# Optimization experiments

Measured on AMD Instinct MI355X. Metric: run time of the kernel, lower is better.

The kernel has to match this reference:

```python
import jax, jax.numpy as jnp
import numpy as np

KERNEL_BW = 0.4  # RBF (Laplacian) kernel bandwidth from the original code


def setup_inputs() -> dict:
    key = jax.random.key(0)
    k1, k2 = jax.random.split(key)
    N, C = 8192, 1000
    inp = jax.random.normal(k1, (N, C), dtype=jnp.float32)
    target = jax.random.randint(k2, (N,), 0, C, dtype=jnp.int64)
    return {"input": inp, "target": target}


def reference(input, target):
    # input: [N, C] logits; target: [N] int labels
    target = target.reshape(-1)
    probs = jax.nn.softmax(input, axis=1)
    predicted_probs = jnp.max(probs, axis=1)           # [N] confidence p_i
    pred_labels = jnp.argmax(probs, axis=1)            # [N]
    correct_mask = (pred_labels == target).astype(predicted_probs.dtype)  # [N]
    c_minus_r = correct_mask - predicted_probs          # [N]
    # Pairwise terms: dot[i,j] = (c_i - p_i)(c_j - p_j); k[i,j] = exp(-|p_i - p_j| / 0.4)
    dot_product = jnp.outer(c_minus_r, c_minus_r)       # [N, N]
    kernel = jnp.exp(-jnp.abs(predicted_probs[:, None] - predicted_probs[None, :]) / KERNEL_BW)
    n = predicted_probs.shape[0]
    return jnp.sum(dot_product * kernel) / jnp.asarray(n, predicted_probs.dtype) ** 2
```

## Files before the change

### kernel.cpp

```cpp
#include <hip/hip_runtime.h>
#include <math.h>
#include <stdint.h>


#define WAVE 64
static constexpr float KBW_INV = 2.5f;

__global__ __launch_bounds__(256) void rowstats_kernel(
    const float* __restrict__ inp, const int* __restrict__ tgt,
    float* __restrict__ P, float* __restrict__ A, float* __restrict__ B,
    int N, int C) {
  const int wave = threadIdx.x >> 6;
  const int lane = threadIdx.x & 63;
  const int row = blockIdx.x * 4 + wave;
  if (row >= N) return;
  const int C4 = C >> 2;
  const float4* rp = reinterpret_cast<const float4*>(inp + (size_t)row * C);

  float4 x[4];
  bool valid[4];
  float m = -INFINITY;
  int am = 0x7fffffff;
  #pragma unroll
  for (int w = 0; w < 4; ++w) {
    const int k = lane + w * WAVE;
    valid[w] = (k < C4);
    if (valid[w]) {
      float4 v = rp[k];
      x[w] = v;
      const int base = k * 4;
      if (v.x > m) { m = v.x; am = base + 0; }
      if (v.y > m) { m = v.y; am = base + 1; }
      if (v.z > m) { m = v.z; am = base + 2; }
      if (v.w > m) { m = v.w; am = base + 3; }
    }
  }
  #pragma unroll
  for (int off = 32; off; off >>= 1) {
    float om = __shfl_xor(m, off);
    int oi = __shfl_xor(am, off);
    if (om > m || (om == m && oi < am)) { m = om; am = oi; }
  }
  float s = 0.f;
  #pragma unroll
  for (int w = 0; w < 4; ++w) {
    if (valid[w]) {
      s += __expf(x[w].x - m) + __expf(x[w].y - m) +
           __expf(x[w].z - m) + __expf(x[w].w - m);
    }
  }
  #pragma unroll
  for (int off = 32; off; off >>= 1) s += __shfl_xor(s, off);

  if (lane == 0) {
    const float p = 1.0f / s;
    const float v = ((tgt[row] == am) ? 1.0f : 0.0f) - p;
    P[row] = p;
    A[row] = v * __expf(-p * KBW_INV);
    B[row] = v * __expf(p * KBW_INV);
  }
}

#define JBLK 256

__global__ __launch_bounds__(256) void pairwise_kernel(
    const float* __restrict__ P, const float* __restrict__ A,
    const float* __restrict__ B, double* __restrict__ partials, int N) {
  __shared__ float sp[JBLK], sa[JBLK], sb[JBLK];
  const int nIB = N / 256;
  const int bi = blockIdx.x % nIB;
  const int bj = blockIdx.x / nIB;
  const int tid = threadIdx.x;

  const int j = bj * JBLK + tid;
  sp[tid] = P[j];
  sa[tid] = A[j];
  sb[tid] = B[j];
  __syncthreads();

  const int i = bi * 256 + tid;
  const float pi = P[i];
  const float ai = A[i];
  const float bi_ = B[i];
  double acc = 0.0;
  #pragma unroll 8
  for (int t = 0; t < JBLK; ++t) {
    const float pj = sp[t];
    const bool c = (pi >= pj);
    const float xx = c ? ai : bi_;
    const float yy = c ? sb[t] : sa[t];
    acc += (double)(xx * yy);
  }
  #pragma unroll
  for (int off = 32; off; off >>= 1) acc += __shfl_xor(acc, off);
  __shared__ double wsum[4];
  if ((tid & 63) == 0) wsum[tid >> 6] = acc;
  __syncthreads();
  if (tid == 0) partials[blockIdx.x] = (wsum[0] + wsum[1]) + (wsum[2] + wsum[3]);
}

__global__ __launch_bounds__(256) void finalize_kernel(
    const double* __restrict__ partials, int nPart, float* __restrict__ out,
    double invN2) {
  double acc = 0.0;
  for (int k = threadIdx.x; k < nPart; k += 256) acc += partials[k];
  #pragma unroll
  for (int off = 32; off; off >>= 1) acc += __shfl_xor(acc, off);
  __shared__ double wsum[4];
  if ((threadIdx.x & 63) == 0) wsum[threadIdx.x >> 6] = acc;
  __syncthreads();
  if (threadIdx.x == 0)
    out[0] = (float)(((wsum[0] + wsum[1]) + (wsum[2] + wsum[3])) * invN2);
}

extern "C" void kernel_launch(void* const* d_in, const int* in_sizes, int n_in,
                              void* d_out, int out_size, void* d_ws, size_t ws_size,
                              hipStream_t stream) {
  const float* inp = (const float*)d_in[0];
  const int* tgt = (const int*)d_in[1];
  const int N = in_sizes[1];
  const int C = in_sizes[0] / N;

  float* P = (float*)d_ws;
  float* A = P + N;
  float* B = A + N;
  double* partials =
      (double*)(((uintptr_t)(B + N) + 15) & ~(uintptr_t)15);

  const int rowBlocks = (N + 3) / 4;
  rowstats_kernel<<<rowBlocks, 256, 0, stream>>>(inp, tgt, P, A, B, N, C);

  const int nIB = N / 256;
  const int nPart = nIB * nIB;
  pairwise_kernel<<<nPart, 256, 0, stream>>>(P, A, B, partials, N);

  finalize_kernel<<<1, 256, 0, stream>>>(partials, nPart, (float*)d_out,
                                         1.0 / ((double)N * (double)N));
}
```

Before: 29.40 us.

## Replace pairwise compare-select with fmed3, register-block rows, fuse finalize via atomics

The pairwise kernel no longer loads P. It uses the identity that min(a_i*b_j, b_i*a_j), clamped against zero via fmed3, selects the correct exp term, and accumulates in float instead of double per term. Each thread now handles 4 rows against 128-column tiles from a packed float2 A/B array. The finalize kernel is removed in favour of a fixed-point 64-bit atomic accumulate with a last-block counter. This cuts double-precision adds, loads and one launch, but float accumulation and fixed-point scaling change numerical precision, and the fmed3 selection relies on sign properties of v.

```diff
diff --git a/kernel.cpp b/kernel.cpp
--- a/kernel.cpp
+++ b/kernel.cpp
@@ -8,8 +8,9 @@
 
 __global__ __launch_bounds__(256) void rowstats_kernel(
     const float* __restrict__ inp, const int* __restrict__ tgt,
-    float* __restrict__ P, float* __restrict__ A, float* __restrict__ B,
-    int N, int C) {
+    float2* __restrict__ AB, unsigned long long* __restrict__ acc,
+    unsigned int* __restrict__ counter, int N, int C) {
+  if (blockIdx.x == 0 && threadIdx.x == 0) { *acc = 0ull; *counter = 0u; }
   const int wave = threadIdx.x >> 6;
   const int lane = threadIdx.x & 63;
   const int row = blockIdx.x * 4 + wave;
@@ -55,62 +56,69 @@
   if (lane == 0) {
     const float p = 1.0f / s;
     const float v = ((tgt[row] == am) ? 1.0f : 0.0f) - p;
-    P[row] = p;
-    A[row] = v * __expf(-p * KBW_INV);
-    B[row] = v * __expf(p * KBW_INV);
+    float2 ab;
+    ab.x = v * __expf(-p * KBW_INV);
+    ab.y = v * __expf(p * KBW_INV);
+    AB[row] = ab;
   }
 }
 
-#define JBLK 256
+#define IPT 4
+#define JBLK 128
+
+static constexpr double FXSCALE = 1073741824.0;
 
 __global__ __launch_bounds__(256) void pairwise_kernel(
-    const float* __restrict__ P, const float* __restrict__ A,
-    const float* __restrict__ B, double* __restrict__ partials, int N) {
-  __shared__ float sp[JBLK], sa[JBLK], sb[JBLK];
-  const int nIB = N / 256;
-  const int bi = blockIdx.x % nIB;
-  const int bj = blockIdx.x / nIB;
+    const float2* __restrict__ AB, unsigned long long* __restrict__ acc,
+    unsigned int* __restrict__ counter, float* __restrict__ out, int N,
+    int nBlocks) {
+  __shared__ float2 sj[JBLK];
+  const int nJB = N / JBLK;
+  const int bi = blockIdx.x / nJB;
+  const int bj = blockIdx.x % nJB;
   const int tid = threadIdx.x;
 
-  const int j = bj * JBLK + tid;
-  sp[tid] = P[j];
-  sa[tid] = A[j];
-  sb[tid] = B[j];
+  if (tid < JBLK) sj[tid] = AB[bj * JBLK + tid];
+
+  float2 abi[IPT];
+  #pragma unroll
+  for (int u = 0; u < IPT; ++u) abi[u] = AB[bi * (256 * IPT) + u * 256 + tid];
   __syncthreads();
 
-  const int i = bi * 256 + tid;
-  const float pi = P[i];
-  const float ai = A[i];
-  const float bi_ = B[i];
-  double acc = 0.0;
+  float facc[IPT];
+  #pragma unroll
+  for (int u = 0; u < IPT; ++u) facc[u] = 0.f;
+
   #pragma unroll 8
   for (int t = 0; t < JBLK; ++t) {
-    const float pj = sp[t];
-    const bool c = (pi >= pj);
-    const float xx = c ? ai : bi_;
-    const float yy = c ? sb[t] : sa[t];
-    acc += (double)(xx * yy);
+    const float aj = sj[t].x;
+    const float bj_ = sj[t].y;
+    #pragma unroll
+    for (int u = 0; u < IPT; ++u) {
+      const float xx = abi[u].x * bj_;
+      const float yy = abi[u].y * aj;
+      facc[u] += __builtin_amdgcn_fmed3f(xx, yy, 0.0f);
+    }
   }
+
+  double dacc = (double)((facc[0] + facc[1]) + (facc[2] + facc[3]));
   #pragma unroll
-  for (int off = 32; off; off >>= 1) acc += __shfl_xor(acc, off);
+  for (int off = 32; off; off >>= 1) dacc += __shfl_xor(dacc, off);
   __shared__ double wsum[4];
-  if ((tid & 63) == 0) wsum[tid >> 6] = acc;
+  if ((tid & 63) == 0) wsum[tid >> 6] = dacc;
   __syncthreads();
-  if (tid == 0) partials[blockIdx.x] = (wsum[0] + wsum[1]) + (wsum[2] + wsum[3]);
-}
-
-__global__ __launch_bounds__(256) void finalize_kernel(
-    const double* __restrict__ partials, int nPart, float* __restrict__ out,
-    double invN2) {
-  double acc = 0.0;
-  for (int k = threadIdx.x; k < nPart; k += 256) acc += partials[k];
-  #pragma unroll
-  for (int off = 32; off; off >>= 1) acc += __shfl_xor(acc, off);
-  __shared__ double wsum[4];
-  if ((threadIdx.x & 63) == 0) wsum[threadIdx.x >> 6] = acc;
-  __syncthreads();
-  if (threadIdx.x == 0)
-    out[0] = (float)(((wsum[0] + wsum[1]) + (wsum[2] + wsum[3])) * invN2);
+  if (tid == 0) {
+    const double blocksum = (wsum[0] + wsum[1]) + (wsum[2] + wsum[3]);
+    const long long fx = __double2ll_rn(blocksum * FXSCALE);
+    atomicAdd(acc, (unsigned long long)fx);
+    __threadfence();
+    const unsigned int done = atomicAdd(counter, 1u);
+    if (done == (unsigned int)nBlocks - 1u) {
+      const unsigned long long total = atomicAdd(acc, 0ull);
+      const double s = (double)(long long)total * (1.0 / FXSCALE);
+      out[0] = (float)(s / ((double)N * (double)N));
+    }
+  }
 }
 
 extern "C" void kernel_launch(void* const* d_in, const int* in_sizes, int n_in,
@@ -121,19 +129,17 @@
   const int N = in_sizes[1];
   const int C = in_sizes[0] / N;
 
-  float* P = (float*)d_ws;
-  float* A = P + N;
-  float* B = A + N;
-  double* partials =
-      (double*)(((uintptr_t)(B + N) + 15) & ~(uintptr_t)15);
+  float2* AB = (float2*)d_ws;
+  unsigned long long* acc =
+      (unsigned long long*)(((uintptr_t)(AB + N) + 15) & ~(uintptr_t)15);
+  unsigned int* counter = (unsigned int*)(acc + 1);
 
   const int rowBlocks = (N + 3) / 4;
-  rowstats_kernel<<<rowBlocks, 256, 0, stream>>>(inp, tgt, P, A, B, N, C);
+  rowstats_kernel<<<rowBlocks, 256, 0, stream>>>(inp, tgt, AB, acc, counter, N, C);
 
-  const int nIB = N / 256;
-  const int nPart = nIB * nIB;
-  pairwise_kernel<<<nPart, 256, 0, stream>>>(P, A, B, partials, N);
-
-  finalize_kernel<<<1, 256, 0, stream>>>(partials, nPart, (float*)d_out,
-                                         1.0 / ((double)N * (double)N));
+  const int nIB = N / (256 * IPT);
+  const int nJB = N / JBLK;
+  const int nPair = nIB * nJB;
+  pairwise_kernel<<<nPair, 256, 0, stream>>>(AB, acc, counter, (float*)d_out,
+                                             N, nPair);
 }
```

Result: slower. 30.55 us (+3.9%).
